# Kernel tuning notes

Measured on AMD Instinct MI355X. Metric: run time of the kernel, lower is better.

Reference implementation:

```python
import jax, jax.numpy as jnp
import numpy as np

N_NODES = 50000
N_EDGES = 600000
NODE_DIM = 128
HIDDEN = 128
LN_EPS = 1e-5


def setup_inputs() -> dict:
    key = jax.random.key(0)
    ks = jax.random.split(key, 12)
    x = jax.random.normal(ks[0], (N_NODES, NODE_DIM), dtype=jnp.float32)
    edge_index = jax.random.randint(ks[1], (2, N_EDGES), 0, N_NODES, dtype=jnp.int32)
    # GCNConv weights (glorot-ish scaling)
    W1 = jax.random.normal(ks[2], (NODE_DIM, HIDDEN), dtype=jnp.float32) / np.sqrt(NODE_DIM)
    b1 = jnp.zeros((HIDDEN,), jnp.float32)
    W2 = jax.random.normal(ks[3], (HIDDEN, HIDDEN), dtype=jnp.float32) / np.sqrt(HIDDEN)
    b2 = jnp.zeros((HIDDEN,), jnp.float32)
    g1 = jnp.ones((HIDDEN,), jnp.float32)
    beta1 = jnp.zeros((HIDDEN,), jnp.float32)
    g2 = jnp.ones((HIDDEN,), jnp.float32)
    beta2 = jnp.zeros((HIDDEN,), jnp.float32)
    return {"x": x, "edge_index": edge_index, "W1": W1, "b1": b1, "g1": g1,
            "beta1": beta1, "W2": W2, "b2": b2, "g2": g2, "beta2": beta2}


def _gcn_conv(x, src, dst, norm, W, b, n):
    # x' = sum_{j->i} norm_ji * (x_j @ W) + b   (self-loops already in src/dst)
    h = x @ W                                   # [N, H]
    msg = h[src] * norm[:, None]                # [E+N, H]
    out = jax.ops.segment_sum(msg, dst, num_segments=n)
    return out + b


def _layer_norm(x, gamma, beta):
    mu = jnp.mean(x, axis=-1, keepdims=True)
    var = jnp.mean((x - mu) ** 2, axis=-1, keepdims=True)
    return (x - mu) * jax.lax.rsqrt(var + LN_EPS) * gamma + beta


def reference(x, edge_index, W1, b1, g1, beta1, W2, b2, g2, beta2):
    n = x.shape[0]
    loop = jnp.arange(n, dtype=edge_index.dtype)
    src = jnp.concatenate([edge_index[0], loop])
    dst = jnp.concatenate([edge_index[1], loop])
    # symmetric normalization with self-loops (PyG GCNConv default)
    deg = jax.ops.segment_sum(jnp.ones_like(dst, dtype=x.dtype), dst, num_segments=n)
    dinv = jnp.where(deg > 0, jax.lax.rsqrt(jnp.maximum(deg, 1.0)), 0.0)
    norm = dinv[src] * dinv[dst]                # [E+N]

    h = _gcn_conv(x, src, dst, norm, W1, b1, n)
    h = _layer_norm(h, g1, beta1)
    h = jax.nn.relu(h)                          # relu between layers only
    h = _gcn_conv(h, src, dst, norm, W2, b2, n)
    h = _layer_norm(h, g2, beta2)
    return h
```

## Files before the change

### kernel.cpp

```cpp
#include <hip/hip_runtime.h>

#define DIM 128
#define LN_EPS 1e-5f

typedef __attribute__((ext_vector_type(8))) short bf16x8;
typedef __attribute__((ext_vector_type(4))) float f32x4;

static __device__ __forceinline__ unsigned short f2bf(float f) {
    unsigned int u = __builtin_bit_cast(unsigned int, f);
    u += 0x7fffu + ((u >> 16) & 1u);
    return (unsigned short)(u >> 16);
}
static __device__ __forceinline__ float bf2f_lo(unsigned int u) {
    return __builtin_bit_cast(float, u << 16);
}
static __device__ __forceinline__ float bf2f_hi(unsigned int u) {
    return __builtin_bit_cast(float, u & 0xffff0000u);
}

__global__ __launch_bounds__(256) void wt_count_kernel(const float* __restrict__ W1,
                                                       const float* __restrict__ W2,
                                                       unsigned short* __restrict__ Wt1,
                                                       unsigned short* __restrict__ Wt2,
                                                       const int* __restrict__ dst,
                                                       int* __restrict__ counts, int E) {
    int b = blockIdx.x;
    if (b < 128) {
        int elem = b * 256 + threadIdx.x;
        int which = elem >> 14;
        int rest = elem & 16383;
        int c = rest >> 7;
        int k = rest & 127;
        const float* W = which ? W2 : W1;
        unsigned short* Wt = which ? Wt2 : Wt1;
        Wt[c * 128 + k] = f2bf(W[k * 128 + c]);
    } else {
        int e = (b - 128) * 256 + threadIdx.x;
        if (e < E) atomicAdd(&counts[dst[e]], 1);
    }
}

__global__ __launch_bounds__(256) void scan1_kernel(const int* __restrict__ counts,
                                                    int* __restrict__ tmp,
                                                    int* __restrict__ bsums,
                                                    float* __restrict__ dinv, int n) {
    __shared__ int ts[256];
    int tid = threadIdx.x;
    int base = blockIdx.x * 1024 + tid * 4;
    int v[4];
#pragma unroll
    for (int j = 0; j < 4; ++j) {
        int i = base + j;
        v[j] = (i < n) ? counts[i] : 0;
        if (i < n) dinv[i] = rsqrtf((float)(v[j] + 1));
    }
    int s = v[0] + v[1] + v[2] + v[3];
    ts[tid] = s;
    __syncthreads();
    for (int off = 1; off < 256; off <<= 1) {
        int t2 = (tid >= off) ? ts[tid - off] : 0;
        __syncthreads();
        ts[tid] += t2;
        __syncthreads();
    }
    int excl = ts[tid] - s;
    int pre = excl;
#pragma unroll
    for (int j = 0; j < 4; ++j) {
        int i = base + j;
        if (i < n) tmp[i] = pre;
        pre += v[j];
    }
    if (tid == 255) bsums[blockIdx.x] = ts[255];
}

__global__ __launch_bounds__(256) void scan3_kernel(const int* __restrict__ tmp,
                                                    const int* __restrict__ bsums,
                                                    int* __restrict__ rowptr,
                                                    int* __restrict__ cursor,
                                                    int n, int E, int nb) {
    __shared__ int s_add;
    if (threadIdx.x < 64) {
        int lane = threadIdx.x;
        int v = (lane < nb) ? bsums[lane] : 0;
        int x = v;
#pragma unroll
        for (int off = 1; off < 64; off <<= 1) {
            int y = __shfl_up(x, off);
            if (lane >= off) x += y;
        }
        int excl = x - v;
        int mine = __builtin_amdgcn_readlane(excl, blockIdx.x);
        if (lane == 0) s_add = mine;
    }
    __syncthreads();
    int add = s_add;
    int base = blockIdx.x * 1024 + threadIdx.x * 4;
#pragma unroll
    for (int j = 0; j < 4; ++j) {
        int i = base + j;
        if (i < n) {
            int val = tmp[i] + add;
            rowptr[i] = val;
            cursor[i] = val;
        }
    }
    if (blockIdx.x == 0 && threadIdx.x == 0) rowptr[n] = E;
}

__global__ __launch_bounds__(256) void fill_kernel(const int* __restrict__ src,
                                                   const int* __restrict__ dst,
                                                   int* __restrict__ cursor,
                                                   unsigned short* __restrict__ colsrc, int E) {
    int e = blockIdx.x * 256 + threadIdx.x;
    if (e < E) {
        int p = atomicAdd(&cursor[dst[e]], 1);
        colsrc[p] = (unsigned short)src[e];
    }
}

__global__ __launch_bounds__(256) void gemm_mfma_f32_kernel(const float* __restrict__ A,
                                                            const unsigned short* __restrict__ Bt,
                                                            const float* __restrict__ dinv,
                                                            unsigned short* __restrict__ H,
                                                            int n, int ntiles) {
    __shared__ unsigned short Wlds[128 * 136];
    for (int u = threadIdx.x; u < 2048; u += 256) {
        int row = u >> 4;
        int sub = u & 15;
        *(bf16x8*)&Wlds[row * 136 + sub * 8] = *(const bf16x8*)(Bt + row * 128 + sub * 8);
    }
    __syncthreads();

    int wid = threadIdx.x >> 6;
    int lane = threadIdx.x & 63;
    int tile = blockIdx.x * 4 + wid;
    if (tile >= ntiles) tile = ntiles - 1;
    int r0 = tile * 16;
    int mrow = lane & 15;
    int kgrp = lane >> 4;

    int arow_i = r0 + mrow;
    if (arow_i > n - 1) arow_i = n - 1;
    const float* arow = A + (size_t)arow_i * DIM + kgrp * 8;

    f32x4 acc[8];
#pragma unroll
    for (int t = 0; t < 8; ++t) acc[t] = (f32x4){0.f, 0.f, 0.f, 0.f};

#pragma unroll
    for (int kc = 0; kc < 4; ++kc) {
        float4 v0 = *(const float4*)(arow + kc * 32);
        float4 v1 = *(const float4*)(arow + kc * 32 + 4);
        bf16x8 af;
        af[0] = (short)f2bf(v0.x); af[1] = (short)f2bf(v0.y);
        af[2] = (short)f2bf(v0.z); af[3] = (short)f2bf(v0.w);
        af[4] = (short)f2bf(v1.x); af[5] = (short)f2bf(v1.y);
        af[6] = (short)f2bf(v1.z); af[7] = (short)f2bf(v1.w);
#pragma unroll
        for (int t = 0; t < 8; ++t) {
            bf16x8 bfv = *(const bf16x8*)&Wlds[(t * 16 + mrow) * 136 + kc * 32 + kgrp * 8];
            acc[t] = __builtin_amdgcn_mfma_f32_16x16x32_bf16(af, bfv, acc[t], 0, 0, 0);
        }
    }

    float dv[4];
#pragma unroll
    for (int reg = 0; reg < 4; ++reg) {
        int rr = r0 + kgrp * 4 + reg;
        dv[reg] = (rr < n) ? dinv[rr] : 0.f;
    }
#pragma unroll
    for (int t = 0; t < 8; ++t) {
#pragma unroll
        for (int reg = 0; reg < 4; ++reg) {
            int row = r0 + kgrp * 4 + reg;
            if (row < n) {
                int col = t * 16 + mrow;
                H[(size_t)row * DIM + col] = f2bf(acc[t][reg] * dv[reg]);
            }
        }
    }
}

__global__ __launch_bounds__(256) void gemm_mfma_kernel(const unsigned short* __restrict__ A,
                                                        const unsigned short* __restrict__ Bt,
                                                        const float* __restrict__ dinv,
                                                        unsigned short* __restrict__ H,
                                                        int n, int ntiles) {
    __shared__ unsigned short Wlds[128 * 136];
    for (int u = threadIdx.x; u < 2048; u += 256) {
        int row = u >> 4;
        int sub = u & 15;
        *(bf16x8*)&Wlds[row * 136 + sub * 8] = *(const bf16x8*)(Bt + row * 128 + sub * 8);
    }
    __syncthreads();

    int wid = threadIdx.x >> 6;
    int lane = threadIdx.x & 63;
    int tile = blockIdx.x * 4 + wid;
    if (tile >= ntiles) tile = ntiles - 1;
    int r0 = tile * 16;
    int mrow = lane & 15;
    int kgrp = lane >> 4;

    int arow_i = r0 + mrow;
    if (arow_i > n - 1) arow_i = n - 1;
    const unsigned short* arow = A + (size_t)arow_i * DIM + kgrp * 8;

    f32x4 acc[8];
#pragma unroll
    for (int t = 0; t < 8; ++t) acc[t] = (f32x4){0.f, 0.f, 0.f, 0.f};

#pragma unroll
    for (int kc = 0; kc < 4; ++kc) {
        bf16x8 af = *(const bf16x8*)(arow + kc * 32);
#pragma unroll
        for (int t = 0; t < 8; ++t) {
            bf16x8 bfv = *(const bf16x8*)&Wlds[(t * 16 + mrow) * 136 + kc * 32 + kgrp * 8];
            acc[t] = __builtin_amdgcn_mfma_f32_16x16x32_bf16(af, bfv, acc[t], 0, 0, 0);
        }
    }

    float dv[4];
#pragma unroll
    for (int reg = 0; reg < 4; ++reg) {
        int rr = r0 + kgrp * 4 + reg;
        dv[reg] = (rr < n) ? dinv[rr] : 0.f;
    }
#pragma unroll
    for (int t = 0; t < 8; ++t) {
#pragma unroll
        for (int reg = 0; reg < 4; ++reg) {
            int row = r0 + kgrp * 4 + reg;
            if (row < n) {
                int col = t * 16 + mrow;
                H[(size_t)row * DIM + col] = f2bf(acc[t][reg] * dv[reg]);
            }
        }
    }
}

__global__ __launch_bounds__(256) void gather_ln_kernel(const int* __restrict__ rowptr,
                                                        const unsigned short* __restrict__ colsrc,
                                                        const uint2* __restrict__ H2,
                                                        const float* __restrict__ dinv,
                                                        const float* __restrict__ bias,
                                                        const float* __restrict__ gamma,
                                                        const float* __restrict__ beta,
                                                        uint2* __restrict__ out_bf,
                                                        float* __restrict__ out_f,
                                                        int n, int relu) {
    int wid = threadIdx.x >> 6;
    int lane = threadIdx.x & 63;
    int half = lane >> 5;
    int hl = lane & 31;
    int r = blockIdx.x * 8 + wid * 2 + half;
    int valid = (r < n);
    int rc = valid ? r : (n - 1);

    float di = dinv[rc];
    float4 bb = ((const float4*)bias)[hl];
    float4 gg = ((const float4*)gamma)[hl];
    float4 be = ((const float4*)beta)[hl];

    uint2 su = H2[(size_t)rc * 32 + hl];
    float a0 = bf2f_lo(su.x), a1 = bf2f_hi(su.x);
    float a2 = bf2f_lo(su.y), a3 = bf2f_hi(su.y);

    int p0 = rowptr[rc];
    int p1 = rowptr[rc + 1];
    int deg = p1 - p0;
    int maxd = max(deg, __shfl_xor(deg, 32));
    int nchunks = (maxd + 15) >> 4;
    int hbase = half << 5;

    for (int c = 0; c < nchunks; ++c) {
        int cbase = c * 16;
        int gi = p0 + cbase + hl;
        gi = gi < p1 ? gi : p1 - 1;
        int idxv = (int)colsrc[gi];

        uint2 h[16];
#pragma unroll
        for (int j = 0; j < 16; ++j) {
            int s = __shfl(idxv, hbase + j);
            h[j] = H2[(size_t)s * 32 + hl];
        }
#pragma unroll
        for (int j = 0; j < 16; ++j) {
            bool act = (cbase + j < deg);
            a0 += act ? bf2f_lo(h[j].x) : 0.f;
            a1 += act ? bf2f_hi(h[j].x) : 0.f;
            a2 += act ? bf2f_lo(h[j].y) : 0.f;
            a3 += act ? bf2f_hi(h[j].y) : 0.f;
        }
    }

    float v0 = a0 * di + bb.x;
    float v1 = a1 * di + bb.y;
    float v2 = a2 * di + bb.z;
    float v3 = a3 * di + bb.w;

    float s1 = v0 + v1 + v2 + v3;
    float s2 = v0 * v0 + v1 * v1 + v2 * v2 + v3 * v3;
#pragma unroll
    for (int off = 16; off > 0; off >>= 1) {
        s1 += __shfl_xor(s1, off);
        s2 += __shfl_xor(s2, off);
    }
    float mu = s1 * (1.f / 128.f);
    float var = s2 * (1.f / 128.f) - mu * mu;
    float rstd = rsqrtf(var + LN_EPS);

    float o0 = (v0 - mu) * rstd * gg.x + be.x;
    float o1 = (v1 - mu) * rstd * gg.y + be.y;
    float o2 = (v2 - mu) * rstd * gg.z + be.z;
    float o3 = (v3 - mu) * rstd * gg.w + be.w;
    if (relu) {
        o0 = fmaxf(o0, 0.f); o1 = fmaxf(o1, 0.f);
        o2 = fmaxf(o2, 0.f); o3 = fmaxf(o3, 0.f);
    }
    if (valid) {
        if (out_bf) {
            uint2 pk;
            pk.x = (unsigned int)f2bf(o0) | ((unsigned int)f2bf(o1) << 16);
            pk.y = (unsigned int)f2bf(o2) | ((unsigned int)f2bf(o3) << 16);
            out_bf[(size_t)r * 32 + hl] = pk;
        } else {
            ((float4*)out_f)[(size_t)r * 32 + hl] = make_float4(o0, o1, o2, o3);
        }
    }
}

extern "C" void kernel_launch(void* const* d_in, const int* in_sizes, int n_in,
                              void* d_out, int out_size, void* d_ws, size_t ws_size,
                              hipStream_t stream) {
    const float* x   = (const float*)d_in[0];
    const int*   ei  = (const int*)d_in[1];
    const float* W1  = (const float*)d_in[2];
    const float* b1  = (const float*)d_in[3];
    const float* g1  = (const float*)d_in[4];
    const float* be1 = (const float*)d_in[5];
    const float* W2  = (const float*)d_in[6];
    const float* b2  = (const float*)d_in[7];
    const float* g2  = (const float*)d_in[8];
    const float* be2 = (const float*)d_in[9];

    int n = in_sizes[0] / DIM;
    int E = in_sizes[1] / 2;
    const int* src = ei;
    const int* dst = ei + E;

    char* wp = (char*)d_ws;
    auto alloc = [&](size_t bytes) {
        void* p = (void*)wp;
        wp += (bytes + 255) & ~(size_t)255;
        return p;
    };
    float*          dinv   = (float*)alloc((size_t)n * 4);
    int*            counts = (int*)alloc((size_t)n * 4);
    int*            tmp    = (int*)alloc((size_t)n * 4);
    int*            rowptr = (int*)alloc((size_t)(n + 1) * 4);
    int*            cursor = (int*)alloc((size_t)n * 4);
    int*            bsums  = (int*)alloc(64 * 4);
    unsigned short* colsrc = (unsigned short*)alloc((size_t)E * 2);
    unsigned short* Wt1    = (unsigned short*)alloc(128 * 128 * 2);
    unsigned short* Wt2    = (unsigned short*)alloc(128 * 128 * 2);
    unsigned short* H      = (unsigned short*)alloc((size_t)n * DIM * 2);
    unsigned short* Y1     = (unsigned short*)alloc((size_t)n * DIM * 2);

    hipMemsetAsync(counts, 0, (size_t)n * 4, stream);

    int gE = (E + 255) / 256;
    wt_count_kernel<<<128 + gE, 256, 0, stream>>>(W1, W2, Wt1, Wt2, dst, counts, E);

    int nb1 = (n + 1023) / 1024;
    scan1_kernel<<<nb1, 256, 0, stream>>>(counts, tmp, bsums, dinv, n);
    scan3_kernel<<<nb1, 256, 0, stream>>>(tmp, bsums, rowptr, cursor, n, E, nb1);
    fill_kernel<<<gE, 256, 0, stream>>>(src, dst, cursor, colsrc, E);

    int ntiles = (n + 15) / 16;
    int gG = (ntiles + 3) / 4;
    int gA = (n + 7) / 8;

    gemm_mfma_f32_kernel<<<gG, 256, 0, stream>>>(x, Wt1, dinv, H, n, ntiles);
    gather_ln_kernel<<<gA, 256, 0, stream>>>(rowptr, colsrc, (const uint2*)H, dinv,
                                             b1, g1, be1, (uint2*)Y1, nullptr, n, 1);

    gemm_mfma_kernel<<<gG, 256, 0, stream>>>(Y1, Wt2, dinv, H, n, ntiles);
    gather_ln_kernel<<<gA, 256, 0, stream>>>(rowptr, colsrc, (const uint2*)H, dinv,
                                             b2, g2, be2, nullptr, (float*)d_out, n, 0);
}
```

Before: 231.7 us.

## Fuse CSR fill into first GEMM and first gather-LN into second GEMM

The CSR fill work now runs as extra blocks inside the first GEMM launch, so the two independent tasks share one grid. The first aggregation, LayerNorm and ReLU are fused into the second GEMM: each wave gathers neighbor rows for 16 nodes, normalizes them, stages the bf16 result in LDS and feeds it to MFMA, so the Y1 intermediate is never written to or read from global memory. In exchange the fused gather runs with fewer waves than the standalone gather kernel and uses more LDS per block, which may limit occupancy for the latency-bound gather.

Measured after the change: 233.4 us. About the same (+0.7%).

```diff
diff --git a/kernel.cpp b/kernel.cpp
--- a/kernel.cpp
+++ b/kernel.cpp
@@ -108,23 +108,25 @@
     if (blockIdx.x == 0 && threadIdx.x == 0) rowptr[n] = E;
 }
 
-__global__ __launch_bounds__(256) void fill_kernel(const int* __restrict__ src,
-                                                   const int* __restrict__ dst,
-                                                   int* __restrict__ cursor,
-                                                   unsigned short* __restrict__ colsrc, int E) {
-    int e = blockIdx.x * 256 + threadIdx.x;
-    if (e < E) {
-        int p = atomicAdd(&cursor[dst[e]], 1);
-        colsrc[p] = (unsigned short)src[e];
-    }
-}
-
-__global__ __launch_bounds__(256) void gemm_mfma_f32_kernel(const float* __restrict__ A,
-                                                            const unsigned short* __restrict__ Bt,
-                                                            const float* __restrict__ dinv,
-                                                            unsigned short* __restrict__ H,
-                                                            int n, int ntiles) {
+__global__ __launch_bounds__(256) void gemm1_fill_kernel(const float* __restrict__ A,
+                                                         const unsigned short* __restrict__ Bt,
+                                                         const float* __restrict__ dinv,
+                                                         unsigned short* __restrict__ H,
+                                                         int n, int ntiles, int gG,
+                                                         const int* __restrict__ src,
+                                                         const int* __restrict__ dst,
+                                                         int* __restrict__ cursor,
+                                                         unsigned short* __restrict__ colsrc,
+                                                         int E) {
     __shared__ unsigned short Wlds[128 * 136];
+    if (blockIdx.x >= gG) {
+        int e = (blockIdx.x - gG) * 256 + threadIdx.x;
+        if (e < E) {
+            int p = atomicAdd(&cursor[dst[e]], 1);
+            colsrc[p] = (unsigned short)src[e];
+        }
+        return;
+    }
     for (int u = threadIdx.x; u < 2048; u += 256) {
         int row = u >> 4;
         int sub = u & 15;
@@ -183,16 +185,22 @@
     }
 }
 
-__global__ __launch_bounds__(256) void gemm_mfma_kernel(const unsigned short* __restrict__ A,
-                                                        const unsigned short* __restrict__ Bt,
-                                                        const float* __restrict__ dinv,
-                                                        unsigned short* __restrict__ H,
-                                                        int n, int ntiles) {
+__global__ __launch_bounds__(256) void gather_gemm_kernel(const int* __restrict__ rowptr,
+                                                          const unsigned short* __restrict__ colsrc,
+                                                          const uint4* __restrict__ H4,
+                                                          const float* __restrict__ dinv,
+                                                          const float* __restrict__ bias,
+                                                          const float* __restrict__ gamma,
+                                                          const float* __restrict__ beta,
+                                                          const unsigned short* __restrict__ Wt2,
+                                                          unsigned short* __restrict__ H2,
+                                                          int n, int ntiles) {
     __shared__ unsigned short Wlds[128 * 136];
+    __shared__ unsigned short Tl[4][16][136];
     for (int u = threadIdx.x; u < 2048; u += 256) {
         int row = u >> 4;
         int sub = u & 15;
-        *(bf16x8*)&Wlds[row * 136 + sub * 8] = *(const bf16x8*)(Bt + row * 128 + sub * 8);
+        *(bf16x8*)&Wlds[row * 136 + sub * 8] = *(const bf16x8*)(Wt2 + row * 128 + sub * 8);
     }
     __syncthreads();
 
@@ -201,23 +209,111 @@
     int tile = blockIdx.x * 4 + wid;
     if (tile >= ntiles) tile = ntiles - 1;
     int r0 = tile * 16;
+    int grp = lane >> 4;
+    int gl = lane & 15;
+
+    float4 bb0 = ((const float4*)bias)[gl * 2];
+    float4 bb1 = ((const float4*)bias)[gl * 2 + 1];
+    float4 gg0 = ((const float4*)gamma)[gl * 2];
+    float4 gg1 = ((const float4*)gamma)[gl * 2 + 1];
+    float4 be0 = ((const float4*)beta)[gl * 2];
+    float4 be1 = ((const float4*)beta)[gl * 2 + 1];
+
+    for (int t = 0; t < 4; ++t) {
+        int r = r0 + t * 4 + grp;
+        int rc = (r < n) ? r : (n - 1);
+        float di = dinv[rc];
+        uint4 su = H4[(size_t)rc * 16 + gl];
+        float a0 = bf2f_lo(su.x), a1 = bf2f_hi(su.x);
+        float a2 = bf2f_lo(su.y), a3 = bf2f_hi(su.y);
+        float a4 = bf2f_lo(su.z), a5 = bf2f_hi(su.z);
+        float a6 = bf2f_lo(su.w), a7 = bf2f_hi(su.w);
+
+        int p0 = rowptr[rc];
+        int p1 = rowptr[rc + 1];
+        int deg = p1 - p0;
+        int m = max(deg, __shfl_xor(deg, 16));
+        m = max(m, __shfl_xor(m, 32));
+        int nch = (m + 15) >> 4;
+
+        for (int c = 0; c < nch; ++c) {
+            int cb = c * 16;
+            int gi = p0 + cb + gl;
+            gi = gi < p1 ? gi : p1 - 1;
+            int idxv = (int)colsrc[gi];
+
+            uint4 h[16];
+#pragma unroll
+            for (int j = 0; j < 16; ++j) {
+                int s = __shfl(idxv, grp * 16 + j);
+                h[j] = H4[(size_t)s * 16 + gl];
+            }
+#pragma unroll
+            for (int j = 0; j < 16; ++j) {
+                bool act = (cb + j < deg);
+                a0 += act ? bf2f_lo(h[j].x) : 0.f;
+                a1 += act ? bf2f_hi(h[j].x) : 0.f;
+                a2 += act ? bf2f_lo(h[j].y) : 0.f;
+                a3 += act ? bf2f_hi(h[j].y) : 0.f;
+                a4 += act ? bf2f_lo(h[j].z) : 0.f;
+                a5 += act ? bf2f_hi(h[j].z) : 0.f;
+                a6 += act ? bf2f_lo(h[j].w) : 0.f;
+                a7 += act ? bf2f_hi(h[j].w) : 0.f;
+            }
+        }
+
+        float v0 = a0 * di + bb0.x;
+        float v1 = a1 * di + bb0.y;
+        float v2 = a2 * di + bb0.z;
+        float v3 = a3 * di + bb0.w;
+        float v4 = a4 * di + bb1.x;
+        float v5 = a5 * di + bb1.y;
+        float v6 = a6 * di + bb1.z;
+        float v7 = a7 * di + bb1.w;
+
+        float s1 = v0 + v1 + v2 + v3 + v4 + v5 + v6 + v7;
+        float s2 = v0 * v0 + v1 * v1 + v2 * v2 + v3 * v3 +
+                   v4 * v4 + v5 * v5 + v6 * v6 + v7 * v7;
+#pragma unroll
+        for (int off = 8; off > 0; off >>= 1) {
+            s1 += __shfl_xor(s1, off);
+            s2 += __shfl_xor(s2, off);
+        }
+        float mu = s1 * (1.f / 128.f);
+        float var = s2 * (1.f / 128.f) - mu * mu;
+        float rstd = rsqrtf(var + LN_EPS);
+
+        float o0 = fmaxf((v0 - mu) * rstd * gg0.x + be0.x, 0.f);
+        float o1 = fmaxf((v1 - mu) * rstd * gg0.y + be0.y, 0.f);
+        float o2 = fmaxf((v2 - mu) * rstd * gg0.z + be0.z, 0.f);
+        float o3 = fmaxf((v3 - mu) * rstd * gg0.w + be0.w, 0.f);
+        float o4 = fmaxf((v4 - mu) * rstd * gg1.x + be1.x, 0.f);
+        float o5 = fmaxf((v5 - mu) * rstd * gg1.y + be1.y, 0.f);
+        float o6 = fmaxf((v6 - mu) * rstd * gg1.z + be1.z, 0.f);
+        float o7 = fmaxf((v7 - mu) * rstd * gg1.w + be1.w, 0.f);
+
+        bf16x8 pk;
+        pk[0] = (short)f2bf(o0); pk[1] = (short)f2bf(o1);
+        pk[2] = (short)f2bf(o2); pk[3] = (short)f2bf(o3);
+        pk[4] = (short)f2bf(o4); pk[5] = (short)f2bf(o5);
+        pk[6] = (short)f2bf(o6); pk[7] = (short)f2bf(o7);
+        *(bf16x8*)&Tl[wid][t * 4 + grp][gl * 8] = pk;
+    }
+
+    __syncthreads();
+
     int mrow = lane & 15;
-    int kgrp = lane >> 4;
-
-    int arow_i = r0 + mrow;
-    if (arow_i > n - 1) arow_i = n - 1;
-    const unsigned short* arow = A + (size_t)arow_i * DIM + kgrp * 8;
-
+    int kg = lane >> 4;
     f32x4 acc[8];
 #pragma unroll
     for (int t = 0; t < 8; ++t) acc[t] = (f32x4){0.f, 0.f, 0.f, 0.f};
 
 #pragma unroll
     for (int kc = 0; kc < 4; ++kc) {
-        bf16x8 af = *(const bf16x8*)(arow + kc * 32);
+        bf16x8 af = *(const bf16x8*)&Tl[wid][mrow][kc * 32 + kg * 8];
 #pragma unroll
         for (int t = 0; t < 8; ++t) {
-            bf16x8 bfv = *(const bf16x8*)&Wlds[(t * 16 + mrow) * 136 + kc * 32 + kgrp * 8];
+            bf16x8 bfv = *(const bf16x8*)&Wlds[(t * 16 + mrow) * 136 + kc * 32 + kg * 8];
             acc[t] = __builtin_amdgcn_mfma_f32_16x16x32_bf16(af, bfv, acc[t], 0, 0, 0);
         }
     }
@@ -225,17 +321,17 @@
     float dv[4];
 #pragma unroll
     for (int reg = 0; reg < 4; ++reg) {
-        int rr = r0 + kgrp * 4 + reg;
+        int rr = r0 + kg * 4 + reg;
         dv[reg] = (rr < n) ? dinv[rr] : 0.f;
     }
 #pragma unroll
     for (int t = 0; t < 8; ++t) {
 #pragma unroll
         for (int reg = 0; reg < 4; ++reg) {
-            int row = r0 + kgrp * 4 + reg;
+            int row = r0 + kg * 4 + reg;
             if (row < n) {
                 int col = t * 16 + mrow;
-                H[(size_t)row * DIM + col] = f2bf(acc[t][reg] * dv[reg]);
+                H2[(size_t)row * DIM + col] = f2bf(acc[t][reg] * dv[reg]);
             }
         }
     }
@@ -368,7 +464,7 @@
     unsigned short* Wt1    = (unsigned short*)alloc(128 * 128 * 2);
     unsigned short* Wt2    = (unsigned short*)alloc(128 * 128 * 2);
     unsigned short* H      = (unsigned short*)alloc((size_t)n * DIM * 2);
-    unsigned short* Y1     = (unsigned short*)alloc((size_t)n * DIM * 2);
+    unsigned short* H2     = (unsigned short*)alloc((size_t)n * DIM * 2);
 
     hipMemsetAsync(counts, 0, (size_t)n * 4, stream);
 
@@ -378,17 +474,17 @@
     int nb1 = (n + 1023) / 1024;
     scan1_kernel<<<nb1, 256, 0, stream>>>(counts, tmp, bsums, dinv, n);
     scan3_kernel<<<nb1, 256, 0, stream>>>(tmp, bsums, rowptr, cursor, n, E, nb1);
-    fill_kernel<<<gE, 256, 0, stream>>>(src, dst, cursor, colsrc, E);
 
     int ntiles = (n + 15) / 16;
     int gG = (ntiles + 3) / 4;
+
+    gemm1_fill_kernel<<<gG + gE, 256, 0, stream>>>(x, Wt1, dinv, H, n, ntiles, gG,
+                                                   src, dst, cursor, colsrc, E);
+
+    gather_gemm_kernel<<<gG, 256, 0, stream>>>(rowptr, colsrc, (const uint4*)H, dinv,
+                                               b1, g1, be1, Wt2, H2, n, ntiles);
+
     int gA = (n + 7) / 8;
-
-    gemm_mfma_f32_kernel<<<gG, 256, 0, stream>>>(x, Wt1, dinv, H, n, ntiles);
-    gather_ln_kernel<<<gA, 256, 0, stream>>>(rowptr, colsrc, (const uint2*)H, dinv,
-                                             b1, g1, be1, (uint2*)Y1, nullptr, n, 1);
-
-    gemm_mfma_kernel<<<gG, 256, 0, stream>>>(Y1, Wt2, dinv, H, n, ntiles);
-    gather_ln_kernel<<<gA, 256, 0, stream>>>(rowptr, colsrc, (const uint2*)H, dinv,
+    gather_ln_kernel<<<gA, 256, 0, stream>>>(rowptr, colsrc, (const uint2*)H2, dinv,
                                              b2, g2, be2, nullptr, (float*)d_out, n, 0);
 }
```
